# Kernel optimization log

Measured on AMD Instinct MI355X. Metric: run time of the kernel, lower is better.

Reference implementation:

```python
import jax, jax.numpy as jnp
import numpy as np

N_HEADS = 16
D_HEAD = 64
IGNORE = -100000.0


def setup_inputs() -> dict:
    key = jax.random.key(0)
    ks = jax.random.split(key, 5)
    B, S, D = 2, 2048, 1024
    return {
        "residual": jax.random.normal(ks[0], (B, S, D), dtype=jnp.float32),
        "q": jax.random.normal(ks[1], (B, S, D), dtype=jnp.float32),
        "k": jax.random.normal(ks[2], (B, S, D), dtype=jnp.float32),
        "v": jax.random.normal(ks[3], (B, S, D), dtype=jnp.float32),
        "W_O": jax.random.normal(ks[4], (N_HEADS, D_HEAD, D), dtype=jnp.float32) * 0.02,
        "b_O": jnp.zeros((D,), dtype=jnp.float32),
    }


def reference(residual, q, k, v, W_O, b_O):
    B, S, _ = q.shape
    attn_scale = np.sqrt(D_HEAD).astype(np.float32)  # use_attn_scale=True
    # split heads: [..., pos, (h d)] -> [..., pos, h, d]
    qh = q.reshape(B, S, N_HEADS, D_HEAD)
    kh = k.reshape(B, S, N_HEADS, D_HEAD)
    vh = v.reshape(B, S, N_HEADS, D_HEAD)
    # scores: [..., head, query_pos, key_pos]
    scores = jnp.einsum("bqhd,bkhd->bhqk", qh, kh) / attn_scale
    causal = jnp.tril(jnp.ones((S, S), dtype=bool))
    scores = jnp.where(causal, scores, jnp.float32(IGNORE))
    pattern = jax.nn.softmax(scores, axis=-1)
    # weighted sum of values: [..., query_pos, head, d_head]
    z = jnp.einsum("bkhd,bhqk->bqhd", vh, pattern)
    out = jnp.einsum("bqhd,hdm->bqm", z, W_O) + b_O
    return (residual, out)
```

## Files before the change

kernel.cpp:

```cpp
#include <hip/hip_runtime.h>

#define B_ 2
#define S_ 2048
#define D_ 1024
#define H_ 16
#define DH_ 64
#define NP_ 2048

typedef short v8s __attribute__((ext_vector_type(8)));
typedef float v4f __attribute__((ext_vector_type(4)));
typedef float v16f __attribute__((ext_vector_type(16)));
typedef unsigned int v2u __attribute__((ext_vector_type(2)));
typedef unsigned int v4u __attribute__((ext_vector_type(4)));
typedef unsigned int uint32;

__device__ inline short f2bf(float f) {
  unsigned u = __float_as_uint(f);
  u = (u + 0x7FFFu + ((u >> 16) & 1u)) >> 16;
  return (short)u;
}

__device__ inline unsigned pk_bf16(float lo, float hi) {
  unsigned r;
  asm("v_cvt_pk_bf16_f32 %0, %1, %2" : "=v"(r) : "v"(lo), "v"(hi));
  return r;
}

__device__ inline void gll16(const void* g, void* l) {
  __builtin_amdgcn_global_load_lds(
      (const __attribute__((address_space(1))) void*)g,
      (__attribute__((address_space(3))) void*)l, 16, 0, 0);
}

__global__ __launch_bounds__(256) void cvt_all_kernel(
    const float* __restrict__ k, short* __restrict__ kb,
    const float* __restrict__ v, short* __restrict__ vt,
    const float* __restrict__ w, short* __restrict__ wt) {
  __shared__ short t[64][64 + 8];
  int bid = blockIdx.x;
  int tid = threadIdx.x;
  if (bid < 2048) {
    int i = bid * 256 + tid;
    float4 a = ((const float4*)k)[2 * i];
    float4 b = ((const float4*)k)[2 * i + 1];
    v8s o;
    o[0] = f2bf(a.x); o[1] = f2bf(a.y); o[2] = f2bf(a.z); o[3] = f2bf(a.w);
    o[4] = f2bf(b.x); o[5] = f2bf(b.y); o[6] = f2bf(b.z); o[7] = f2bf(b.w);
    ((v8s*)kb)[i] = o;
    return;
  }
  int r = tid >> 2, c16 = (tid & 3) * 16;
  if (bid < 3072) {
    int id = bid - 2048;
    int st = id & 31;
    int bh = id >> 5;
    int b = bh >> 4, h = bh & 15;
    const float* vp = v + ((size_t)(b * S_ + st * 64 + r)) * D_ + h * DH_ + c16;
    for (int i = 0; i < 16; i += 4) {
      float4 a = *(const float4*)(vp + i);
      t[r][c16 + i + 0] = f2bf(a.x);
      t[r][c16 + i + 1] = f2bf(a.y);
      t[r][c16 + i + 2] = f2bf(a.z);
      t[r][c16 + i + 3] = f2bf(a.w);
    }
    __syncthreads();
    short* op = vt + ((size_t)((b * H_ + h) * DH_ + r)) * S_ + st * 64 + c16;
    v8s o0, o1;
    for (int j = 0; j < 8; ++j) { o0[j] = t[c16 + j][r]; o1[j] = t[c16 + 8 + j][r]; }
    *(v8s*)op = o0;
    *(v8s*)(op + 8) = o1;
  } else {
    int id = bid - 3072;
    int tk = id & 15, tm = id >> 4;
    const float* wp = w + (size_t)(tk * 64 + r) * D_ + tm * 64 + c16;
    for (int i = 0; i < 16; i += 4) {
      float4 a = *(const float4*)(wp + i);
      t[r][c16 + i + 0] = f2bf(a.x);
      t[r][c16 + i + 1] = f2bf(a.y);
      t[r][c16 + i + 2] = f2bf(a.z);
      t[r][c16 + i + 3] = f2bf(a.w);
    }
    __syncthreads();
    short* op = wt + (size_t)(tm * 64 + r) * D_ + tk * 64 + c16;
    v8s o0, o1;
    for (int j = 0; j < 8; ++j) { o0[j] = t[c16 + j][r]; o1[j] = t[c16 + 8 + j][r]; }
    *(v8s*)op = o0;
    *(v8s*)(op + 8) = o1;
  }
}

template <int SPLITS>
__global__ __launch_bounds__(256, 4) void attn_kernel(
    const float* __restrict__ q, const short* __restrict__ kbf,
    const short* __restrict__ vtb, uint32* __restrict__ Opart,
    float* __restrict__ Lsum, const float* __restrict__ residual,
    float* __restrict__ res_out) {
  int bid = blockIdx.x;
  int bh = bid & 31;
  int sp = (SPLITS == 2) ? ((bid >> 5) & 1) : 0;
  int t = (SPLITS == 2) ? (bid >> 6) : (bid >> 5);
  int g = t >> 2;
  int qt = (g == 0) ? 15 - t : (g == 1) ? t - 4 : (g == 2) ? 19 - t : t - 8;
  int b = bh >> 4, h = bh & 15;

  const int nt = 2 * qt + 2;
  const int t0 = (SPLITS == 2 && sp == 1) ? qt + 1 : 0;
  const int t1 = (SPLITS == 2 && sp == 0) ? qt : nt - 1;

  int tid = threadIdx.x;
  int wave = tid >> 6, lane = tid & 63;
  int l31 = lane & 31, h32 = lane >> 5;

  __shared__ short Klds[64][64];
  __shared__ short Vlds[64][64];

  const int qrow0 = qt * 128 + wave * 32;
  const int lr8 = lane >> 3;
  const int scol = ((lane & 7) ^ lr8) << 3;

  const int sw = wave & 1;
  const short* pk_ = kbf + (size_t)b * S_ * D_ + h * DH_ +
                     (size_t)(t0 * 64 + sw * 8 + lr8) * D_ + scol;
  const short* pv_ = vtb + (size_t)(b * H_ + h) * DH_ * S_ +
                     (size_t)(sw * 8 + lr8) * S_ + t0 * 64 + scol;

  v8s qf[4];
  {
    const float* qp = q + (size_t)(b * S_ + qrow0 + l31) * D_ + h * DH_ + h32 * 8;
    const float sc = 0.125f * 1.44269504f;
#pragma unroll
    for (int d4 = 0; d4 < 4; ++d4) {
      float4 x = *(const float4*)(qp + d4 * 16);
      float4 y = *(const float4*)(qp + d4 * 16 + 4);
      v8s tq;
      tq[0] = f2bf(x.x * sc); tq[1] = f2bf(x.y * sc);
      tq[2] = f2bf(x.z * sc); tq[3] = f2bf(x.w * sc);
      tq[4] = f2bf(y.x * sc); tq[5] = f2bf(y.y * sc);
      tq[6] = f2bf(y.z * sc); tq[7] = f2bf(y.w * sc);
      qf[d4] = tq;
    }
  }

  v16f O0, O1;
#pragma unroll
  for (int r = 0; r < 16; ++r) { O0[r] = 0.f; O1[r] = 0.f; }
  float L = 0.f;
  const int swz = (l31 & 7) << 3;

  for (int s = t0; s <= t1; ++s) {
    if (wave < 2) {
#pragma unroll
      for (int i = 0; i < 4; ++i)
        gll16(pk_ + (size_t)(i * 16) * D_, &Klds[i * 16 + sw * 8][0]);
    } else {
#pragma unroll
      for (int i = 0; i < 4; ++i)
        gll16(pv_ + (size_t)(i * 16) * S_, &Vlds[i * 16 + sw * 8][0]);
    }
    pk_ += (size_t)64 * D_;
    pv_ += 64;
    asm volatile("s_waitcnt vmcnt(0)" ::: "memory");
    __builtin_amdgcn_sched_barrier(0);
    __builtin_amdgcn_s_barrier();
    __builtin_amdgcn_sched_barrier(0);

    int kb = s * 64;
    bool fullskip = (kb >= qrow0 + 32);
    if (!fullskip) {
      bool skip1 = (kb >= qrow0);
      bool msk = (kb + 63 > qrow0);

      __builtin_amdgcn_s_setprio(1);
      v16f S0, S1;
#pragma unroll
      for (int r = 0; r < 16; ++r) { S0[r] = 0.f; S1[r] = 0.f; }
#pragma unroll
      for (int d4 = 0; d4 < 4; ++d4) {
        v8s kf = *(const v8s*)&Klds[l31][(((d4 << 1) | h32) << 3) ^ swz];
        S0 = __builtin_amdgcn_mfma_f32_32x32x16_bf16(kf, qf[d4], S0, 0, 0, 0);
      }
      if (!skip1) {
#pragma unroll
        for (int d4 = 0; d4 < 4; ++d4) {
          v8s kf = *(const v8s*)&Klds[32 + l31][(((d4 << 1) | h32) << 3) ^ swz];
          S1 = __builtin_amdgcn_mfma_f32_32x32x16_bf16(kf, qf[d4], S1, 0, 0, 0);
        }
      }
      __builtin_amdgcn_s_setprio(0);

      int qg = qrow0 + l31;
      if (msk) {
#pragma unroll
        for (int r = 0; r < 16; ++r) {
          int kl = kb + (r & 3) + 8 * (r >> 2) + 4 * h32;
          if (kl > qg) S0[r] = -1e30f;
        }
        if (!skip1) {
#pragma unroll
          for (int r = 0; r < 16; ++r) {
            int kl = kb + 32 + (r & 3) + 8 * (r >> 2) + 4 * h32;
            if (kl > qg) S1[r] = -1e30f;
          }
        }
      }

      float rs = 0.f;
      unsigned pw0[8], pw1[8];
#pragma unroll
      for (int r = 0; r < 16; ++r) {
        S0[r] = __builtin_amdgcn_exp2f(S0[r]);
        rs += S0[r];
      }
#pragma unroll
      for (int w = 0; w < 8; ++w) pw0[w] = pk_bf16(S0[2 * w], S0[2 * w + 1]);
      if (!skip1) {
#pragma unroll
        for (int r = 0; r < 16; ++r) {
          S1[r] = __builtin_amdgcn_exp2f(S1[r]);
          rs += S1[r];
        }
#pragma unroll
        for (int w = 0; w < 8; ++w) pw1[w] = pk_bf16(S1[2 * w], S1[2 * w + 1]);
      }
      rs += __shfl_xor(rs, 32);
      L += rs;

      __builtin_amdgcn_s_setprio(1);
#pragma unroll
      for (int ks = 0; ks < 2; ++ks) {
        v2u a = __builtin_amdgcn_permlane32_swap(pw0[ks * 4 + 0], pw0[ks * 4 + 2], false, false);
        v2u c = __builtin_amdgcn_permlane32_swap(pw0[ks * 4 + 1], pw0[ks * 4 + 3], false, false);
        v4u fw; fw.x = a.x; fw.y = c.x; fw.z = a.y; fw.w = c.y;
        v8s pb = __builtin_bit_cast(v8s, fw);
        v8s vf0 = *(const v8s*)&Vlds[l31][(((ks << 1) | h32) << 3) ^ swz];
        O0 = __builtin_amdgcn_mfma_f32_32x32x16_bf16(vf0, pb, O0, 0, 0, 0);
        v8s vf1 = *(const v8s*)&Vlds[32 + l31][(((ks << 1) | h32) << 3) ^ swz];
        O1 = __builtin_amdgcn_mfma_f32_32x32x16_bf16(vf1, pb, O1, 0, 0, 0);
      }
      if (!skip1) {
#pragma unroll
        for (int ks = 0; ks < 2; ++ks) {
          v2u a = __builtin_amdgcn_permlane32_swap(pw1[ks * 4 + 0], pw1[ks * 4 + 2], false, false);
          v2u c = __builtin_amdgcn_permlane32_swap(pw1[ks * 4 + 1], pw1[ks * 4 + 3], false, false);
          v4u fw; fw.x = a.x; fw.y = c.x; fw.z = a.y; fw.w = c.y;
          v8s pb = __builtin_bit_cast(v8s, fw);
          v8s vf0 = *(const v8s*)&Vlds[l31][((((ks + 2) << 1) | h32) << 3) ^ swz];
          O0 = __builtin_amdgcn_mfma_f32_32x32x16_bf16(vf0, pb, O0, 0, 0, 0);
          v8s vf1 = *(const v8s*)&Vlds[32 + l31][((((ks + 2) << 1) | h32) << 3) ^ swz];
          O1 = __builtin_amdgcn_mfma_f32_32x32x16_bf16(vf1, pb, O1, 0, 0, 0);
        }
      }
      __builtin_amdgcn_s_setprio(0);
    }

    __builtin_amdgcn_sched_barrier(0);
    __builtin_amdgcn_s_barrier();
    __builtin_amdgcn_sched_barrier(0);
  }

  int p = bh * 64 + qt * 4 + wave;
  uint32* Op = Opart + ((size_t)(sp * NP_ + p)) * 1024;
#pragma unroll
  for (int w = 0; w < 8; ++w) {
    int dpair = 4 * (w >> 1) + (w & 1) + 2 * h32;
    Op[dpair * 32 + l31] = pk_bf16(O0[2 * w], O0[2 * w + 1]);
    Op[(16 + dpair) * 32 + l31] = pk_bf16(O1[2 * w], O1[2 * w + 1]);
  }
  if (h32 == 0) Lsum[(size_t)(sp * NP_ + p) * 32 + l31] = L;

  {
    constexpr int F4 = (SPLITS == 2) ? 4 : 8;
    const float4* rs_ = (const float4*)residual;
    float4* rd_ = (float4*)res_out;
    size_t base = (size_t)bid * (256 * F4) + tid;
#pragma unroll
    for (int j = 0; j < F4; ++j) rd_[base + j * 256] = rs_[base + j * 256];
  }
}

template <int SPLITS>
__global__ __launch_bounds__(128) void merge_kernel(
    const uint32* __restrict__ Opart, const float* __restrict__ Lsum,
    short* __restrict__ z) {
  int p = blockIdx.x;
  int tid = threadIdx.x;
  int qq = tid & 31, g = tid >> 5;

  float Lt = Lsum[(size_t)p * 32 + qq];
  if constexpr (SPLITS == 2) Lt += Lsum[((size_t)NP_ + p) * 32 + qq];
  float f = 1.f / Lt;

  __shared__ uint32 T[32][33];
#pragma unroll
  for (int j = 0; j < 8; ++j) {
    int dp = g * 8 + j;
    uint32 u0 = Opart[(size_t)p * 1024 + dp * 32 + qq];
    float lo = __uint_as_float(u0 << 16);
    float hi = __uint_as_float(u0 & 0xFFFF0000u);
    if constexpr (SPLITS == 2) {
      uint32 u1 = Opart[((size_t)NP_ + p) * 1024 + dp * 32 + qq];
      lo += __uint_as_float(u1 << 16);
      hi += __uint_as_float(u1 & 0xFFFF0000u);
    }
    T[qq][dp] = pk_bf16(lo * f, hi * f);
  }
  __syncthreads();
  int q2 = tid >> 2, c = (tid & 3) * 8;
  int srow = (p & 63) * 32 + q2;
  int b = p >> 10, h = (p >> 6) & 15;
  uint32* zp = (uint32*)z + ((size_t)(b * S_ + srow)) * (D_ / 2) + h * 32 + c;
#pragma unroll
  for (int j = 0; j < 8; ++j) zp[j] = T[q2][c + j];
}

__global__ __launch_bounds__(256) void proj_kernel(
    const short* __restrict__ z, const short* __restrict__ wt,
    const float* __restrict__ bias, float* __restrict__ out) {
  int bid = blockIdx.x;
  int bm = bid & 31, bn = bid >> 5;
  int tid = threadIdx.x;
  int wave = tid >> 6, lane = tid & 63, lh = lane >> 4, ll = lane & 15;
  int wr = wave >> 1, wc = wave & 1;

  __shared__ short Al[2][128][64];
  __shared__ short Bl[2][128][64];

  const int r8 = lane >> 3;
  const int scol = ((lane & 7) ^ r8) << 3;

  v4f acc[4][4];
#pragma unroll
  for (int m = 0; m < 4; ++m)
#pragma unroll
    for (int n = 0; n < 4; ++n) acc[m][n] = (v4f){0.f, 0.f, 0.f, 0.f};

  auto stage = [&](int kb, int bbuf) {
#pragma unroll
    for (int i = 0; i < 4; ++i) {
      int c = wave * 4 + i;
      gll16(z + (size_t)(bm * 128 + c * 8 + r8) * D_ + kb + scol, &Al[bbuf][c * 8][0]);
    }
#pragma unroll
    for (int i = 0; i < 4; ++i) {
      int c = wave * 4 + i;
      gll16(wt + (size_t)(bn * 128 + c * 8 + r8) * D_ + kb + scol, &Bl[bbuf][c * 8][0]);
    }
  };

  stage(0, 0);
  __syncthreads();

  for (int kt = 0; kt < D_ / 64; ++kt) {
    int bbuf = kt & 1;
    if (kt + 1 < D_ / 64) stage((kt + 1) * 64, bbuf ^ 1);
    v8s af[4][2], bf[4][2];
#pragma unroll
    for (int m = 0; m < 4; ++m) {
      int row = wr * 64 + m * 16 + ll;
#pragma unroll
      for (int c = 0; c < 2; ++c)
        af[m][c] = *(const v8s*)&Al[bbuf][row][(((c << 2) | lh) ^ (ll & 7)) << 3];
    }
#pragma unroll
    for (int n = 0; n < 4; ++n) {
      int row = wc * 64 + n * 16 + ll;
#pragma unroll
      for (int c = 0; c < 2; ++c)
        bf[n][c] = *(const v8s*)&Bl[bbuf][row][(((c << 2) | lh) ^ (ll & 7)) << 3];
    }
#pragma unroll
    for (int m = 0; m < 4; ++m)
#pragma unroll
      for (int n = 0; n < 4; ++n)
#pragma unroll
        for (int c = 0; c < 2; ++c)
          acc[m][n] = __builtin_amdgcn_mfma_f32_16x16x32_bf16(af[m][c], bf[n][c], acc[m][n], 0, 0, 0);
    __syncthreads();
  }

#pragma unroll
  for (int m = 0; m < 4; ++m) {
    int gr = bm * 128 + wr * 64 + m * 16 + lh * 4;
#pragma unroll
    for (int n = 0; n < 4; ++n) {
      int gc = bn * 128 + wc * 64 + n * 16 + ll;
      float bo = bias[gc];
#pragma unroll
      for (int r = 0; r < 4; ++r)
        out[(size_t)(gr + r) * D_ + gc] = acc[m][n][r] + bo;
    }
  }
}

extern "C" void kernel_launch(void* const* d_in, const int* in_sizes, int n_in,
                              void* d_out, int out_size, void* d_ws, size_t ws_size,
                              hipStream_t stream) {
  const float* residual = (const float*)d_in[0];
  const float* q = (const float*)d_in[1];
  const float* k = (const float*)d_in[2];
  const float* v = (const float*)d_in[3];
  const float* W = (const float*)d_in[4];
  const float* bO = (const float*)d_in[5];
  float* out = (float*)d_out;

  const size_t half = (size_t)B_ * S_ * D_;
  char* ws = (char*)d_ws;
  short* kbf = (short*)ws;
  short* vtb = kbf + half;
  short* wtb = vtb + half;
  char* pbase = (char*)(wtb + (size_t)D_ * D_);
  const size_t opart_b = (size_t)NP_ * 1024 * 4;
  const size_t l_b = (size_t)NP_ * 32 * 4;
  const size_t base_b = (size_t)pbase - (size_t)ws;
  short* z = kbf;

  cvt_all_kernel<<<3328, 256, 0, stream>>>(k, kbf, v, vtb, W, wtb);

  if (ws_size >= base_b + 2 * (opart_b + l_b)) {
    uint32* Opart = (uint32*)pbase;
    float* Lsum = (float*)(pbase + 2 * opart_b);
    attn_kernel<2><<<1024, 256, 0, stream>>>(q, kbf, vtb, Opart, Lsum, residual, out);
    merge_kernel<2><<<NP_, 128, 0, stream>>>(Opart, Lsum, z);
  } else {
    uint32* Opart = (uint32*)pbase;
    float* Lsum = (float*)(pbase + opart_b);
    attn_kernel<1><<<512, 256, 0, stream>>>(q, kbf, vtb, Opart, Lsum, residual, out);
    merge_kernel<1><<<NP_, 128, 0, stream>>>(Opart, Lsum, z);
  }
  proj_kernel<<<256, 256, 0, stream>>>(z, wtb, bO, out + half);
}
```

Measured before the change: 70.79 us.

## Use 512-thread attention blocks with 256-row query tiles and four-way KV split

Each attention block now has 8 waves covering 256 query rows, so every K/V tile loaded into LDS is reused by twice as many waves. The KV range is split into four equal segments instead of two, and the merge kernel now sums all splits generically. This halves per-query-row LDS staging traffic and balances causal work across splits. In exchange it adds partial-output traffic and merge cost, and larger blocks may lower occupancy and raise barrier stalls.

New measurement: 84.96 us. 1.2x slower.

```diff
diff --git a/kernel.cpp b/kernel.cpp
--- a/kernel.cpp
+++ b/kernel.cpp
@@ -90,22 +90,22 @@
 }
 
 template <int SPLITS>
-__global__ __launch_bounds__(256, 4) void attn_kernel(
+__global__ __launch_bounds__(512, 4) void attn_kernel(
     const float* __restrict__ q, const short* __restrict__ kbf,
     const short* __restrict__ vtb, uint32* __restrict__ Opart,
     float* __restrict__ Lsum, const float* __restrict__ residual,
     float* __restrict__ res_out) {
   int bid = blockIdx.x;
   int bh = bid & 31;
-  int sp = (SPLITS == 2) ? ((bid >> 5) & 1) : 0;
-  int t = (SPLITS == 2) ? (bid >> 6) : (bid >> 5);
-  int g = t >> 2;
-  int qt = (g == 0) ? 15 - t : (g == 1) ? t - 4 : (g == 2) ? 19 - t : t - 8;
+  int sidx = bid >> 5;
+  int g = sidx >> 3, s = sidx & 7;
+  int qt = (g & 1) ? s : 7 - s;
+  int sp = g;
   int b = bh >> 4, h = bh & 15;
 
-  const int nt = 2 * qt + 2;
-  const int t0 = (SPLITS == 2 && sp == 1) ? qt + 1 : 0;
-  const int t1 = (SPLITS == 2 && sp == 0) ? qt : nt - 1;
+  const int seg = (4 * (qt + 1)) / SPLITS;
+  const int t0 = sp * seg;
+  const int t1 = t0 + seg - 1;
 
   int tid = threadIdx.x;
   int wave = tid >> 6, lane = tid & 63;
@@ -114,11 +114,11 @@
   __shared__ short Klds[64][64];
   __shared__ short Vlds[64][64];
 
-  const int qrow0 = qt * 128 + wave * 32;
+  const int qrow0 = qt * 256 + wave * 32;
   const int lr8 = lane >> 3;
   const int scol = ((lane & 7) ^ lr8) << 3;
 
-  const int sw = wave & 1;
+  const int sw = wave & 3;
   const short* pk_ = kbf + (size_t)b * S_ * D_ + h * DH_ +
                      (size_t)(t0 * 64 + sw * 8 + lr8) * D_ + scol;
   const short* pv_ = vtb + (size_t)(b * H_ + h) * DH_ * S_ +
@@ -147,15 +147,13 @@
   float L = 0.f;
   const int swz = (l31 & 7) << 3;
 
-  for (int s = t0; s <= t1; ++s) {
-    if (wave < 2) {
-#pragma unroll
-      for (int i = 0; i < 4; ++i)
-        gll16(pk_ + (size_t)(i * 16) * D_, &Klds[i * 16 + sw * 8][0]);
+  for (int ss = t0; ss <= t1; ++ss) {
+    if (wave < 4) {
+      gll16(pk_, &Klds[sw * 8][0]);
+      gll16(pk_ + (size_t)32 * D_, &Klds[32 + sw * 8][0]);
     } else {
-#pragma unroll
-      for (int i = 0; i < 4; ++i)
-        gll16(pv_ + (size_t)(i * 16) * S_, &Vlds[i * 16 + sw * 8][0]);
+      gll16(pv_, &Vlds[sw * 8][0]);
+      gll16(pv_ + (size_t)32 * S_, &Vlds[32 + sw * 8][0]);
     }
     pk_ += (size_t)64 * D_;
     pv_ += 64;
@@ -164,7 +162,7 @@
     __builtin_amdgcn_s_barrier();
     __builtin_amdgcn_sched_barrier(0);
 
-    int kb = s * 64;
+    int kb = ss * 64;
     bool fullskip = (kb >= qrow0 + 32);
     if (!fullskip) {
       bool skip1 = (kb >= qrow0);
@@ -258,7 +256,7 @@
     __builtin_amdgcn_sched_barrier(0);
   }
 
-  int p = bh * 64 + qt * 4 + wave;
+  int p = bh * 64 + qt * 8 + wave;
   uint32* Op = Opart + ((size_t)(sp * NP_ + p)) * 1024;
 #pragma unroll
   for (int w = 0; w < 8; ++w) {
@@ -269,12 +267,12 @@
   if (h32 == 0) Lsum[(size_t)(sp * NP_ + p) * 32 + l31] = L;
 
   {
-    constexpr int F4 = (SPLITS == 2) ? 4 : 8;
+    constexpr int NBLK = 32 * 8 * SPLITS;
     const float4* rs_ = (const float4*)residual;
     float4* rd_ = (float4*)res_out;
-    size_t base = (size_t)bid * (256 * F4) + tid;
-#pragma unroll
-    for (int j = 0; j < F4; ++j) rd_[base + j * 256] = rs_[base + j * 256];
+    for (size_t idx = (size_t)bid * 512 + tid; idx < 1048576;
+         idx += (size_t)NBLK * 512)
+      rd_[idx] = rs_[idx];
   }
 }
 
@@ -286,21 +284,22 @@
   int tid = threadIdx.x;
   int qq = tid & 31, g = tid >> 5;
 
-  float Lt = Lsum[(size_t)p * 32 + qq];
-  if constexpr (SPLITS == 2) Lt += Lsum[((size_t)NP_ + p) * 32 + qq];
+  float Lt = 0.f;
+#pragma unroll
+  for (int sp = 0; sp < SPLITS; ++sp)
+    Lt += Lsum[((size_t)sp * NP_ + p) * 32 + qq];
   float f = 1.f / Lt;
 
   __shared__ uint32 T[32][33];
 #pragma unroll
   for (int j = 0; j < 8; ++j) {
     int dp = g * 8 + j;
-    uint32 u0 = Opart[(size_t)p * 1024 + dp * 32 + qq];
-    float lo = __uint_as_float(u0 << 16);
-    float hi = __uint_as_float(u0 & 0xFFFF0000u);
-    if constexpr (SPLITS == 2) {
-      uint32 u1 = Opart[((size_t)NP_ + p) * 1024 + dp * 32 + qq];
-      lo += __uint_as_float(u1 << 16);
-      hi += __uint_as_float(u1 & 0xFFFF0000u);
+    float lo = 0.f, hi = 0.f;
+#pragma unroll
+    for (int sp = 0; sp < SPLITS; ++sp) {
+      uint32 u = Opart[((size_t)sp * NP_ + p) * 1024 + dp * 32 + qq];
+      lo += __uint_as_float(u << 16);
+      hi += __uint_as_float(u & 0xFFFF0000u);
     }
     T[qq][dp] = pk_bf16(lo * f, hi * f);
   }
@@ -416,16 +415,16 @@
 
   cvt_all_kernel<<<3328, 256, 0, stream>>>(k, kbf, v, vtb, W, wtb);
 
-  if (ws_size >= base_b + 2 * (opart_b + l_b)) {
+  if (ws_size >= base_b + 4 * (opart_b + l_b)) {
+    uint32* Opart = (uint32*)pbase;
+    float* Lsum = (float*)(pbase + 4 * opart_b);
+    attn_kernel<4><<<1024, 512, 0, stream>>>(q, kbf, vtb, Opart, Lsum, residual, out);
+    merge_kernel<4><<<NP_, 128, 0, stream>>>(Opart, Lsum, z);
+  } else {
     uint32* Opart = (uint32*)pbase;
     float* Lsum = (float*)(pbase + 2 * opart_b);
-    attn_kernel<2><<<1024, 256, 0, stream>>>(q, kbf, vtb, Opart, Lsum, residual, out);
+    attn_kernel<2><<<512, 512, 0, stream>>>(q, kbf, vtb, Opart, Lsum, residual, out);
     merge_kernel<2><<<NP_, 128, 0, stream>>>(Opart, Lsum, z);
-  } else {
-    uint32* Opart = (uint32*)pbase;
-    float* Lsum = (float*)(pbase + opart_b);
-    attn_kernel<1><<<512, 256, 0, stream>>>(q, kbf, vtb, Opart, Lsum, residual, out);
-    merge_kernel<1><<<NP_, 128, 0, stream>>>(Opart, Lsum, z);
   }
   proj_kernel<<<256, 256, 0, stream>>>(z, wtb, bO, out + half);
 }
```

## Double-buffer K/V tiles in LDS to prefetch next tile during compute

Applied to the files above, without the earlier changes.

K and V tiles are staged into two alternating LDS buffers, and the load for the next key tile is issued before computing on the current one. A partial vmcnt wait lets the current tile's loads complete while the next tile's loads stay in flight. This hides global-to-LDS latency behind the MFMA and softmax work. The cost is doubled LDS use, which could lower occupancy, plus extra address arithmetic.

Measured after the change: 68.31 us (median of 2 runs). -3.5%, faster.

```diff
diff --git a/kernel.cpp b/kernel.cpp
--- a/kernel.cpp
+++ b/kernel.cpp
@@ -111,18 +111,18 @@
   int wave = tid >> 6, lane = tid & 63;
   int l31 = lane & 31, h32 = lane >> 5;
 
-  __shared__ short Klds[64][64];
-  __shared__ short Vlds[64][64];
+  __shared__ short Klds[2][64][64];
+  __shared__ short Vlds[2][64][64];
 
   const int qrow0 = qt * 128 + wave * 32;
   const int lr8 = lane >> 3;
   const int scol = ((lane & 7) ^ lr8) << 3;
 
   const int sw = wave & 1;
-  const short* pk_ = kbf + (size_t)b * S_ * D_ + h * DH_ +
-                     (size_t)(t0 * 64 + sw * 8 + lr8) * D_ + scol;
-  const short* pv_ = vtb + (size_t)(b * H_ + h) * DH_ * S_ +
-                     (size_t)(sw * 8 + lr8) * S_ + t0 * 64 + scol;
+  const short* kbase = kbf + (size_t)b * S_ * D_ + h * DH_ +
+                       (size_t)(sw * 8 + lr8) * D_ + scol;
+  const short* vbase = vtb + (size_t)(b * H_ + h) * DH_ * S_ +
+                       (size_t)(sw * 8 + lr8) * S_ + scol;
 
   v8s qf[4];
   {
@@ -147,19 +147,30 @@
   float L = 0.f;
   const int swz = (l31 & 7) << 3;
 
+  auto stage = [&](int tt, int buf) {
+    if (wave < 2) {
+      const short* kp = kbase + (size_t)(tt * 64) * D_;
+#pragma unroll
+      for (int i = 0; i < 4; ++i)
+        gll16(kp + (size_t)(i * 16) * D_, &Klds[buf][i * 16 + sw * 8][0]);
+    } else {
+      const short* vp = vbase + tt * 64;
+#pragma unroll
+      for (int i = 0; i < 4; ++i)
+        gll16(vp + (size_t)(i * 16) * S_, &Vlds[buf][i * 16 + sw * 8][0]);
+    }
+  };
+
+  stage(t0, t0 & 1);
+
   for (int s = t0; s <= t1; ++s) {
-    if (wave < 2) {
-#pragma unroll
-      for (int i = 0; i < 4; ++i)
-        gll16(pk_ + (size_t)(i * 16) * D_, &Klds[i * 16 + sw * 8][0]);
+    int cur = s & 1;
+    if (s < t1) {
+      stage(s + 1, cur ^ 1);
+      asm volatile("s_waitcnt vmcnt(4)" ::: "memory");
     } else {
-#pragma unroll
-      for (int i = 0; i < 4; ++i)
-        gll16(pv_ + (size_t)(i * 16) * S_, &Vlds[i * 16 + sw * 8][0]);
-    }
-    pk_ += (size_t)64 * D_;
-    pv_ += 64;
-    asm volatile("s_waitcnt vmcnt(0)" ::: "memory");
+      asm volatile("s_waitcnt vmcnt(0)" ::: "memory");
+    }
     __builtin_amdgcn_sched_barrier(0);
     __builtin_amdgcn_s_barrier();
     __builtin_amdgcn_sched_barrier(0);
@@ -176,13 +187,13 @@
       for (int r = 0; r < 16; ++r) { S0[r] = 0.f; S1[r] = 0.f; }
 #pragma unroll
       for (int d4 = 0; d4 < 4; ++d4) {
-        v8s kf = *(const v8s*)&Klds[l31][(((d4 << 1) | h32) << 3) ^ swz];
+        v8s kf = *(const v8s*)&Klds[cur][l31][(((d4 << 1) | h32) << 3) ^ swz];
         S0 = __builtin_amdgcn_mfma_f32_32x32x16_bf16(kf, qf[d4], S0, 0, 0, 0);
       }
       if (!skip1) {
 #pragma unroll
         for (int d4 = 0; d4 < 4; ++d4) {
-          v8s kf = *(const v8s*)&Klds[32 + l31][(((d4 << 1) | h32) << 3) ^ swz];
+          v8s kf = *(const v8s*)&Klds[cur][32 + l31][(((d4 << 1) | h32) << 3) ^ swz];
           S1 = __builtin_amdgcn_mfma_f32_32x32x16_bf16(kf, qf[d4], S1, 0, 0, 0);
         }
       }
@@ -232,9 +243,9 @@
         v2u c = __builtin_amdgcn_permlane32_swap(pw0[ks * 4 + 1], pw0[ks * 4 + 3], false, false);
         v4u fw; fw.x = a.x; fw.y = c.x; fw.z = a.y; fw.w = c.y;
         v8s pb = __builtin_bit_cast(v8s, fw);
-        v8s vf0 = *(const v8s*)&Vlds[l31][(((ks << 1) | h32) << 3) ^ swz];
+        v8s vf0 = *(const v8s*)&Vlds[cur][l31][(((ks << 1) | h32) << 3) ^ swz];
         O0 = __builtin_amdgcn_mfma_f32_32x32x16_bf16(vf0, pb, O0, 0, 0, 0);
-        v8s vf1 = *(const v8s*)&Vlds[32 + l31][(((ks << 1) | h32) << 3) ^ swz];
+        v8s vf1 = *(const v8s*)&Vlds[cur][32 + l31][(((ks << 1) | h32) << 3) ^ swz];
         O1 = __builtin_amdgcn_mfma_f32_32x32x16_bf16(vf1, pb, O1, 0, 0, 0);
       }
       if (!skip1) {
@@ -244,9 +255,9 @@
           v2u c = __builtin_amdgcn_permlane32_swap(pw1[ks * 4 + 1], pw1[ks * 4 + 3], false, false);
           v4u fw; fw.x = a.x; fw.y = c.x; fw.z = a.y; fw.w = c.y;
           v8s pb = __builtin_bit_cast(v8s, fw);
-          v8s vf0 = *(const v8s*)&Vlds[l31][((((ks + 2) << 1) | h32) << 3) ^ swz];
+          v8s vf0 = *(const v8s*)&Vlds[cur][l31][((((ks + 2) << 1) | h32) << 3) ^ swz];
           O0 = __builtin_amdgcn_mfma_f32_32x32x16_bf16(vf0, pb, O0, 0, 0, 0);
-          v8s vf1 = *(const v8s*)&Vlds[32 + l31][((((ks + 2) << 1) | h32) << 3) ^ swz];
+          v8s vf1 = *(const v8s*)&Vlds[cur][32 + l31][((((ks + 2) << 1) | h32) << 3) ^ swz];
           O1 = __builtin_amdgcn_mfma_f32_32x32x16_bf16(vf1, pb, O1, 0, 0, 0);
         }
       }
```
